# Performance work log

Hardware: AMD Instinct MI355X
Metric: run time of the kernel (lower is better)

## Reference

```python
import jax, jax.numpy as jnp
import numpy as np

B, S, D = 2, 2048, 1024
H, DK, DV = 16, 64, 64
DFF = 4096
EPS_RMS = 1e-6


def setup_inputs() -> dict:
    key = jax.random.key(0)
    ks = jax.random.split(key, 10)
    sc = 0.02
    return {
        "x": jax.random.normal(ks[0], (B, S, D), jnp.float32),
        "w_q": jax.random.normal(ks[1], (D, H * DK), jnp.float32) * sc,
        "w_k": jax.random.normal(ks[2], (D, H * DK), jnp.float32) * sc,
        "w_v": jax.random.normal(ks[3], (D, H * DV), jnp.float32) * sc,
        "w_o": jax.random.normal(ks[4], (H * DV, D), jnp.float32) * sc,
        "w_gate": jax.random.normal(ks[5], (D, DFF), jnp.float32) * sc,
        "w_up": jax.random.normal(ks[6], (D, DFF), jnp.float32) * sc,
        "w_down": jax.random.normal(ks[7], (DFF, D), jnp.float32) * sc,
        "g1": jnp.ones((D,), jnp.float32),
        "g2": jnp.ones((D,), jnp.float32),
    }


def _rmsnorm(x, g):
    var = jnp.mean(jnp.square(x), axis=-1, keepdims=True)
    return x * jax.lax.rsqrt(var + EPS_RMS) * g


def _stable_softmax(s):
    # Faithful to source: exp(x) / (sum exp(x) + 1e-9); fully-masked rows -> 0.
    e = jnp.exp(s)
    return e / (jnp.sum(e, axis=-1, keepdims=True) + 1e-9)


def reference(x, w_q, w_k, w_v, w_o, w_gate, w_up, w_down, g1, g2):
    b, s, d = x.shape
    h = _rmsnorm(x, g1)
    q = (h @ w_q).reshape(b, s, H, DK).transpose(0, 2, 1, 3)  # [B,H,S,DK]
    k = (h @ w_k).reshape(b, s, H, DK).transpose(0, 2, 1, 3)
    v = (h @ w_v).reshape(b, s, H, DV).transpose(0, 2, 1, 3)
    scores = jnp.einsum("bhqd,bhkd->bhqk", q, k) / jnp.sqrt(jnp.asarray(DK, x.dtype))
    # triu with diagonal=0: self and future positions are masked
    mask = jnp.triu(jnp.ones((s, s), bool))
    scores = jnp.where(mask, -jnp.inf, scores)
    attn = _stable_softmax(scores)  # [B,H,S,S]
    av = jnp.einsum("bhqk,bhkd->bhqd", attn, v)
    av = av.transpose(0, 2, 1, 3).reshape(b, s, H * DV)
    x = x + av @ w_o  # residual 1
    h2 = _rmsnorm(x, g2)
    hidden = jax.nn.silu(h2 @ w_gate) * (h2 @ w_up)
    return x + hidden @ w_down  # residual 2
```

## Files before the change

### kernel.cpp

```cpp
#include <hip/hip_runtime.h>
#include <cstdint>
#include <cstddef>

typedef unsigned short u16;
typedef unsigned char u8;
typedef unsigned int u32;
typedef __bf16 bf16x8 __attribute__((ext_vector_type(8)));
typedef float floatx4 __attribute__((ext_vector_type(4)));
typedef float floatx16 __attribute__((ext_vector_type(16)));
typedef int i32x8 __attribute__((ext_vector_type(8)));

#define B_ 2
#define S_ 2048
#define D_ 1024
#define H_ 16
#define DFF_ 4096
#define BS_ 4096

__device__ __forceinline__ u16 f2bf(float f) {
  u32 u = __builtin_bit_cast(u32, f);
  u += 0x7fffu + ((u >> 16) & 1u);
  return (u16)(u >> 16);
}
__device__ __forceinline__ float bf2f(u16 h) {
  u32 u = ((u32)h) << 16;
  return __builtin_bit_cast(float, u);
}

__device__ __forceinline__ u32 f2e4m3(float f) {
  u32 u = __builtin_bit_cast(u32, f);
  const u32 s = (u >> 24) & 0x80u;
  const u32 au = u & 0x7fffffffu;
  if (au < 0x3c800000u) return s;
  if (au > 0x43e00000u) return s | 0x7eu;
  const u32 lsb = (au >> 20) & 1u;
  const u32 r = au + 0x0007ffffu + lsb;
  const u32 e = (r >> 23) & 0xffu;
  const u32 m = (r >> 20) & 7u;
  return s | (((e - 120u) & 0xfu) << 3) | m;
}

__device__ __forceinline__ void gl_lds16(const void* g, void* l) {
  __builtin_amdgcn_global_load_lds(
      (const __attribute__((address_space(1))) void*)g,
      (__attribute__((address_space(3))) void*)l, 16, 0, 0);
}

__device__ __forceinline__ void xcd_swz(int GX, int GY, int& bx, int& by) {
  int flat = by * GX + bx;
  const int q = (GX * GY) >> 3;
  flat = (flat & 7) * q + (flat >> 3);
  bx = flat % GX;
  by = flat / GX;
}

__global__ void prep_weights(const float* __restrict__ wq, const float* __restrict__ wk,
                             const float* __restrict__ wv, const float* __restrict__ wo,
                             const float* __restrict__ wg, const float* __restrict__ wu,
                             const float* __restrict__ wd,
                             u16* __restrict__ wqkv_t, u16* __restrict__ wo_t,
                             u8* __restrict__ wguf8, u16* __restrict__ wdn_t) {
  __shared__ float tile[32][33];
  const int id = blockIdx.x;
  const float* src;
  u16* dst = nullptr;
  int R, C, bx, by, mode;
  if (id < 3072) {
    const int which = id >> 10, lo = id & 1023;
    src = which == 0 ? wq : (which == 1 ? wk : wv);
    dst = wqkv_t + which * 1024 * 1024;
    R = 1024; C = 1024; bx = lo & 31; by = lo >> 5; mode = 0;
  } else if (id < 4096) {
    const int lo = id - 3072;
    src = wo; dst = wo_t; R = 1024; C = 1024; bx = lo & 31; by = lo >> 5; mode = 0;
  } else if (id < 8192) {
    const int lo = id - 4096;
    src = wg; R = 1024; C = 4096; bx = lo & 127; by = lo >> 7; mode = 1;
  } else if (id < 12288) {
    const int lo = id - 8192;
    src = wu; R = 1024; C = 4096; bx = lo & 127; by = lo >> 7; mode = 2;
  } else {
    const int lo = id - 12288;
    src = wd; dst = wdn_t; R = 4096; C = 1024; bx = lo & 31; by = lo >> 5; mode = 0;
  }
  const int tx = threadIdx.x, ty = threadIdx.y;
  const int c0 = bx * 32, r0 = by * 32;
#pragma unroll
  for (int i = 0; i < 4; i++)
    tile[ty + i * 8][tx] = src[(size_t)(r0 + ty + i * 8) * C + c0 + tx];
  __syncthreads();
  const int sx = ty * 32 + tx;
  const int oci = sx >> 3, cg = (sx & 7) * 4;
  const int oc = c0 + oci;
  const float v0 = tile[cg][oci], v1 = tile[cg + 1][oci];
  const float v2 = tile[cg + 2][oci], v3 = tile[cg + 3][oci];
  if (mode == 0) {
    uint2 o;
    o.x = (u32)f2bf(v0) | ((u32)f2bf(v1) << 16);
    o.y = (u32)f2bf(v2) | ((u32)f2bf(v3) << 16);
    *(uint2*)(dst + (size_t)oc * R + r0 + cg) = o;
  } else {
    const int orow = (oc >> 5) * 64 + (oc & 31) + (mode == 2 ? 32 : 0);
    const u32 p = f2e4m3(v0 * 64.f) | (f2e4m3(v1 * 64.f) << 8) |
                  (f2e4m3(v2 * 64.f) << 16) | (f2e4m3(v3 * 64.f) << 24);
    *(u32*)(wguf8 + (size_t)orow * 1024 + r0 + cg) = p;
  }
}

template <int F8>
__global__ __launch_bounds__(256) void rmsnorm_kernel(const float* __restrict__ x,
                                                      const float* __restrict__ g,
                                                      void* __restrict__ out) {
  const int row = blockIdx.x, t = threadIdx.x;
  const float4 v = ((const float4*)(x + (size_t)row * 1024))[t];
  float ss = v.x * v.x + v.y * v.y + v.z * v.z + v.w * v.w;
#pragma unroll
  for (int off = 32; off > 0; off >>= 1) ss += __shfl_xor(ss, off);
  __shared__ float red[4];
  if ((t & 63) == 0) red[t >> 6] = ss;
  __syncthreads();
  ss = red[0] + red[1] + red[2] + red[3];
  const float inv = rsqrtf(ss * (1.0f / 1024.0f) + 1e-6f);
  const float4 gv = ((const float4*)g)[t];
  const float y0 = v.x * inv * gv.x, y1 = v.y * inv * gv.y;
  const float y2 = v.z * inv * gv.z, y3 = v.w * inv * gv.w;
  if (F8) {
    const u32 p = f2e4m3(y0) | (f2e4m3(y1) << 8) | (f2e4m3(y2) << 16) | (f2e4m3(y3) << 24);
    ((u32*)out)[(size_t)row * 256 + t] = p;
  } else {
    uint2 o;
    o.x = (u32)f2bf(y0) | ((u32)f2bf(y1) << 16);
    o.y = (u32)f2bf(y2) | ((u32)f2bf(y3) << 16);
    ((uint2*)out)[(size_t)row * 256 + t] = o;
  }
}

template <int BN>
__device__ __forceinline__ void bt_step(const u16* Asb, const u16* Bsb,
                                        floatx16 (&acc)[2][BN / 64],
                                        int wm, int wn, int c31, int khalf) {
  constexpr int NTI = BN / 64;
#pragma unroll
  for (int ks = 0; ks < 4; ks++) {
    bf16x8 af[2], bfr[NTI];
#pragma unroll
    for (int mi = 0; mi < 2; mi++) {
      const int row = wm * 64 + mi * 32 + c31;
      const int e = (ks * 2 + khalf) ^ (row & 7);
      af[mi] = *(const bf16x8*)(Asb + row * 64 + e * 8);
    }
#pragma unroll
    for (int ni = 0; ni < NTI; ni++) {
      const int row = wn * (BN / 2) + ni * 32 + c31;
      const int e = (ks * 2 + khalf) ^ (row & 7);
      bfr[ni] = *(const bf16x8*)(Bsb + row * 64 + e * 8);
    }
#pragma unroll
    for (int mi = 0; mi < 2; mi++)
#pragma unroll
      for (int ni = 0; ni < NTI; ni++)
        acc[mi][ni] = __builtin_amdgcn_mfma_f32_32x32x16_bf16(af[mi], bfr[ni],
                                                              acc[mi][ni], 0, 0, 0);
  }
}

template <int BN, int EPI, int PIPE>
__global__ __launch_bounds__(256) void gemm_bt(const u16* __restrict__ A,
                                               const u16* __restrict__ Bt,
                                               void* __restrict__ Cout,
                                               const float* __restrict__ res,
                                               u16* __restrict__ vTout,
                                               int M, int N, int K) {
  constexpr int NBUF = PIPE ? 2 : 1;
  __shared__ u16 As[NBUF][128 * 64];
  __shared__ u16 Bs[NBUF][BN * 64];
  constexpr int NTI = BN / 64;
  constexpr int NSEG = 16 + BN / 8;
  constexpr int SPW = NSEG / 4;
  const int t = threadIdx.x, w = t >> 6, l = t & 63;

  int bx = (int)blockIdx.x, by = (int)blockIdx.y;
  xcd_swz((int)gridDim.x, (int)gridDim.y, bx, by);
  const int m0 = by * 128, n0 = bx * BN;
  const int wm = w >> 1, wn = w & 1;
  const int c31 = l & 31, khalf = l >> 5;

  const u16* gsrc[SPW];
  u16* ld0[SPW];
  u16* ld1[SPW];
  {
    const int rl = l >> 3, ch = (l & 7) ^ rl;
#pragma unroll
    for (int i = 0; i < SPW; i++) {
      const int s = w * SPW + i;
      if (s < 16) {
        gsrc[i] = A + (size_t)(m0 + s * 8 + rl) * K + ch * 8;
        ld0[i] = As[0] + s * 512;
        ld1[i] = As[NBUF - 1] + s * 512;
      } else {
        gsrc[i] = Bt + (size_t)(n0 + (s - 16) * 8 + rl) * K + ch * 8;
        ld0[i] = Bs[0] + (s - 16) * 512;
        ld1[i] = Bs[NBUF - 1] + (s - 16) * 512;
      }
    }
  }

  floatx16 acc[2][NTI] = {};

  if constexpr (!PIPE) {
    for (int kk = 0; kk < K; kk += 64) {
      __syncthreads();
#pragma unroll
      for (int i = 0; i < SPW; i++) gl_lds16(gsrc[i], ld0[i]);
#pragma unroll
      for (int i = 0; i < SPW; i++) gsrc[i] += 64;
      __syncthreads();
      bt_step<BN>(As[0], Bs[0], acc, wm, wn, c31, khalf);
    }
  } else {
#pragma unroll
    for (int i = 0; i < SPW; i++) gl_lds16(gsrc[i], ld0[i]);
#pragma unroll
    for (int i = 0; i < SPW; i++) gsrc[i] += 64;
    asm volatile("s_waitcnt vmcnt(0)" ::: "memory");
    __builtin_amdgcn_s_barrier();
    for (int kk = 0; kk < K; kk += 128) {
#pragma unroll
      for (int i = 0; i < SPW; i++) gl_lds16(gsrc[i], ld1[i]);
#pragma unroll
      for (int i = 0; i < SPW; i++) gsrc[i] += 64;
      bt_step<BN>(As[0], Bs[0], acc, wm, wn, c31, khalf);
      asm volatile("s_waitcnt vmcnt(0)" ::: "memory");
      __builtin_amdgcn_s_barrier();
      if (kk + 128 < K) {
#pragma unroll
        for (int i = 0; i < SPW; i++) gl_lds16(gsrc[i], ld0[i]);
#pragma unroll
        for (int i = 0; i < SPW; i++) gsrc[i] += 64;
      }
      bt_step<BN>(As[NBUF - 1], Bs[NBUF - 1], acc, wm, wn, c31, khalf);
      asm volatile("s_waitcnt vmcnt(0)" ::: "memory");
      __builtin_amdgcn_s_barrier();
    }
  }

  if constexpr (EPI == 3) {
    if (n0 >= 2048) {
#pragma unroll
      for (int mi = 0; mi < 2; mi++)
#pragma unroll
        for (int ni = 0; ni < NTI; ni++) {
          const int col = n0 + wn * (BN / 2) + ni * 32 + c31 - 2048;
          const int hh = col >> 6, dv = col & 63;
          const int rbase = m0 + wm * 64 + mi * 32 + 4 * khalf;
          const int bb = rbase >> 11;
          u16* vp = vTout + (size_t)((bb * 16 + hh) * 64 + dv) * 2048 + (rbase & 2047);
#pragma unroll
          for (int rg = 0; rg < 4; rg++) {
            uint2 pk;
            pk.x = (u32)f2bf(acc[mi][ni][rg * 4 + 0]) |
                   ((u32)f2bf(acc[mi][ni][rg * 4 + 1]) << 16);
            pk.y = (u32)f2bf(acc[mi][ni][rg * 4 + 2]) |
                   ((u32)f2bf(acc[mi][ni][rg * 4 + 3]) << 16);
            *(uint2*)(vp + rg * 8) = pk;
          }
        }
      return;
    }
  }
#pragma unroll
  for (int mi = 0; mi < 2; mi++)
#pragma unroll
    for (int ni = 0; ni < NTI; ni++) {
      const int col = n0 + wn * (BN / 2) + ni * 32 + c31;
#pragma unroll
      for (int reg = 0; reg < 16; reg++) {
        const int row = m0 + wm * 64 + mi * 32 + (reg & 3) + 8 * (reg >> 2) + 4 * khalf;
        const size_t idx = (size_t)row * N + col;
        if (EPI == 1) ((float*)Cout)[idx] = acc[mi][ni][reg] + res[idx];
        else          ((u16*)Cout)[idx] = f2bf(acc[mi][ni][reg]);
      }
    }
}

__global__ __launch_bounds__(256) void gemm_f8(const u8* __restrict__ A,
                                               const u8* __restrict__ B,
                                               u16* __restrict__ hid,
                                               int M, int K) {
  __shared__ u8 As[128 * 64];
  __shared__ u8 Bs[128 * 64];
  const int t = threadIdx.x, w = t >> 6, l = t & 63;
  int bx = (int)blockIdx.x, by = (int)blockIdx.y;
  xcd_swz((int)gridDim.x, (int)gridDim.y, bx, by);
  const int m0 = by * 128, n0 = bx * 128;
  const int wm = w >> 1, wn = w & 1;
  const int c31 = l & 31, hf = l >> 5;

  const u8* gsrc[4];
  u8* ldst[4];
  {
    const int rl = l >> 2, ch = (l & 3) ^ ((l >> 3) & 3);
#pragma unroll
    for (int i = 0; i < 4; i++) {
      const int s = w * 4 + i;
      if (s < 8) {
        gsrc[i] = A + (size_t)(m0 + s * 16 + rl) * K + ch * 16;
        ldst[i] = As + s * 1024;
      } else {
        gsrc[i] = B + (size_t)(n0 + (s - 8) * 16 + rl) * K + ch * 16;
        ldst[i] = Bs + (s - 8) * 1024;
      }
    }
  }

  floatx16 acc[2][2] = {};

  for (int kk = 0; kk < K; kk += 64) {
    __syncthreads();
#pragma unroll
    for (int i = 0; i < 4; i++) gl_lds16(gsrc[i] + kk, ldst[i]);
    __syncthreads();

    i32x8 af[2], bf[2];
#pragma unroll
    for (int mi = 0; mi < 2; mi++) {
      const int r = wm * 64 + mi * 32 + c31;
      const int g = (r >> 1) & 3;
      const uint4 lo = *(const uint4*)(As + r * 64 + ((2 * hf) ^ g) * 16);
      const uint4 hi = *(const uint4*)(As + r * 64 + ((2 * hf + 1) ^ g) * 16);
      af[mi] = i32x8{(int)lo.x, (int)lo.y, (int)lo.z, (int)lo.w,
                     (int)hi.x, (int)hi.y, (int)hi.z, (int)hi.w};
    }
#pragma unroll
    for (int ni = 0; ni < 2; ni++) {
      const int r = wn * 64 + ni * 32 + c31;
      const int g = (r >> 1) & 3;
      const uint4 lo = *(const uint4*)(Bs + r * 64 + ((2 * hf) ^ g) * 16);
      const uint4 hi = *(const uint4*)(Bs + r * 64 + ((2 * hf + 1) ^ g) * 16);
      bf[ni] = i32x8{(int)lo.x, (int)lo.y, (int)lo.z, (int)lo.w,
                     (int)hi.x, (int)hi.y, (int)hi.z, (int)hi.w};
    }
#pragma unroll
    for (int mi = 0; mi < 2; mi++)
#pragma unroll
      for (int ni = 0; ni < 2; ni++)
        acc[mi][ni] = __builtin_amdgcn_mfma_scale_f32_32x32x64_f8f6f4(
            af[mi], bf[ni], acc[mi][ni], 0, 0,
            0, 0x7F7F7F7F,
            0, 0x79797979);
  }

#pragma unroll
  for (int mi = 0; mi < 2; mi++) {
    const int colo = (bx * 2 + wn) * 32 + c31;
#pragma unroll
    for (int reg = 0; reg < 16; reg++) {
      const int row = m0 + wm * 64 + mi * 32 + (reg & 3) + 8 * (reg >> 2) + 4 * hf;
      const float g = acc[mi][0][reg];
      const float u = acc[mi][1][reg];
      hid[(size_t)row * 4096 + colo] = f2bf(g / (1.f + __expf(-g)) * u);
    }
  }
}

__global__ __launch_bounds__(256) void attn_kernel(const u16* __restrict__ qkv,
                                                   const u16* __restrict__ vT,
                                                   u16* __restrict__ av) {
  __shared__ u16 SM[2 * 8192];
  __shared__ u16 Ps[4 * 2048];
  const int t = threadIdx.x, w = t >> 6, l = t & 63;
  const int lrow = l & 15, lk = l >> 4;
  const int bh = blockIdx.x;
  const int b = bh >> 4, h = bh & 15;
  const int qt = 15 - (int)blockIdx.y;
  const int qbase = qt * 128 + w * 32;
  const int ktmax = 2 * qt + 1;
  u16* Pw = Ps + w * 2048;

  bf16x8 aq[2][2];
#pragma unroll
  for (int sub = 0; sub < 2; sub++)
#pragma unroll
    for (int half = 0; half < 2; half++)
      aq[sub][half] = *(const bf16x8*)(qkv + (size_t)(b * S_ + qbase + sub * 16 + lrow) * 3072 +
                                       h * 64 + half * 32 + lk * 8);

  const u16* gcur[4];
  int gstep[4], loff[4];
#pragma unroll
  for (int i = 0; i < 4; i++) {
    const int c = w + 4 * i;
    const int half = (c >> 2) & 1, grp = c & 3;
    if (c < 8) {
      gcur[i] = qkv + (size_t)(b * S_ + grp * 16 + (l >> 2)) * 3072 + D_ + h * 64 +
                half * 32 + (l & 3) * 8;
      gstep[i] = 64 * 3072;
      loff[i] = half * 2048 + grp * 512;
    } else {
      gcur[i] = vT + (size_t)(bh * 64 + grp * 16 + (l >> 2)) * S_ + half * 32 + (l & 3) * 8;
      gstep[i] = 64;
      loff[i] = 4096 + half * 2048 + grp * 512;
    }
  }

  floatx4 oacc[2][4] = {};
  float den[2] = {0.f, 0.f};

  int cur = 0;
#pragma unroll
  for (int i = 0; i < 4; i++) { gl_lds16(gcur[i], SM + loff[i]); gcur[i] += gstep[i]; }

  for (int kt = 0; kt <= ktmax; kt++) {
    __syncthreads();
    if (kt < ktmax) {
#pragma unroll
      for (int i = 0; i < 4; i++) {
        gl_lds16(gcur[i], SM + (cur ^ 1) * 8192 + loff[i]);
        gcur[i] += gstep[i];
      }
    }
    const u16* Kbuf = SM + cur * 8192;
    const u16* Vbuf = Kbuf + 4096;

    bf16x8 bk[4][2];
#pragma unroll
    for (int ct = 0; ct < 4; ct++)
#pragma unroll
      for (int half = 0; half < 2; half++)
        bk[ct][half] = *(const bf16x8*)(Kbuf + half * 2048 + (ct * 16 + lrow) * 32 + lk * 8);

    floatx4 sf[2][4] = {};
#pragma unroll
    for (int sub = 0; sub < 2; sub++)
#pragma unroll
      for (int ct = 0; ct < 4; ct++) {
        sf[sub][ct] = __builtin_amdgcn_mfma_f32_16x16x32_bf16(bk[ct][0], aq[sub][0],
                                                              sf[sub][ct], 0, 0, 0);
        sf[sub][ct] = __builtin_amdgcn_mfma_f32_16x16x32_bf16(bk[ct][1], aq[sub][1],
                                                              sf[sub][ct], 0, 0, 0);
      }

#pragma unroll
    for (int sub = 0; sub < 2; sub++) {
      const int qp = qbase + sub * 16 + lrow;
      const int prow = sub * 16 + lrow;
#pragma unroll
      for (int ct = 0; ct < 4; ct++) {
        const int kb = kt * 64 + ct * 16 + lk * 4;
        float p0 = (kb + 0 < qp) ? __expf(sf[sub][ct][0] * 0.125f) : 0.f;
        float p1 = (kb + 1 < qp) ? __expf(sf[sub][ct][1] * 0.125f) : 0.f;
        float p2 = (kb + 2 < qp) ? __expf(sf[sub][ct][2] * 0.125f) : 0.f;
        float p3 = (kb + 3 < qp) ? __expf(sf[sub][ct][3] * 0.125f) : 0.f;
        den[sub] += (p0 + p1) + (p2 + p3);
        uint2 pk;
        pk.x = (u32)f2bf(p0) | ((u32)f2bf(p1) << 16);
        pk.y = (u32)f2bf(p2) | ((u32)f2bf(p3) << 16);
        *(uint2*)(Pw + prow * 64 + (((2 * ct + (lk >> 1)) ^ (lrow & 7)) << 3) +
                  (lk & 1) * 4) = pk;
      }
    }

    bf16x8 ap[2][2], bv[4][2];
#pragma unroll
    for (int sub = 0; sub < 2; sub++)
#pragma unroll
      for (int kh = 0; kh < 2; kh++) {
        const int prow = sub * 16 + lrow;
        ap[sub][kh] = *(const bf16x8*)(Pw + prow * 64 + (((kh * 4 + lk) ^ (prow & 7)) << 3));
      }
#pragma unroll
    for (int ni = 0; ni < 4; ni++)
#pragma unroll
      for (int kh = 0; kh < 2; kh++)
        bv[ni][kh] = *(const bf16x8*)(Vbuf + kh * 2048 + (ni * 16 + lrow) * 32 + lk * 8);
#pragma unroll
    for (int sub = 0; sub < 2; sub++)
#pragma unroll
      for (int ni = 0; ni < 4; ni++) {
        oacc[sub][ni] = __builtin_amdgcn_mfma_f32_16x16x32_bf16(ap[sub][0], bv[ni][0],
                                                                oacc[sub][ni], 0, 0, 0);
        oacc[sub][ni] = __builtin_amdgcn_mfma_f32_16x16x32_bf16(ap[sub][1], bv[ni][1],
                                                                oacc[sub][ni], 0, 0, 0);
      }
    cur ^= 1;
  }

#pragma unroll
  for (int sub = 0; sub < 2; sub++) {
    den[sub] += __shfl_xor(den[sub], 16);
    den[sub] += __shfl_xor(den[sub], 32);
  }
  float dq[2][4];
#pragma unroll
  for (int sub = 0; sub < 2; sub++)
#pragma unroll
    for (int r = 0; r < 4; r++)
      dq[sub][r] = __shfl(den[sub], lk * 4 + r);

#pragma unroll
  for (int sub = 0; sub < 2; sub++)
#pragma unroll
    for (int ni = 0; ni < 4; ni++)
#pragma unroll
      for (int r = 0; r < 4; r++) {
        const int row = qbase + sub * 16 + lk * 4 + r;
        const int col = h * 64 + ni * 16 + lrow;
        av[(size_t)(b * S_ + row) * 1024 + col] = f2bf(oacc[sub][ni][r] / (dq[sub][r] + 1e-9f));
      }
}

#define OFF_WQKV 0u
#define OFF_WO   6291456u
#define OFF_WGU8 8388608u
#define OFF_WDN  16777216u
#define OFF_H1   25165824u
#define OFF_QKV  33554432u
#define OFF_VT   58720256u
#define OFF_AV   67108864u
#define OFF_X1   75497472u
#define OFF_H2F8 92274688u
#define OFF_HID  96468992u

extern "C" void kernel_launch(void* const* d_in, const int* in_sizes, int n_in,
                              void* d_out, int out_size, void* d_ws, size_t ws_size,
                              hipStream_t stream) {
  const float* x      = (const float*)d_in[0];
  const float* w_q    = (const float*)d_in[1];
  const float* w_k    = (const float*)d_in[2];
  const float* w_v    = (const float*)d_in[3];
  const float* w_o    = (const float*)d_in[4];
  const float* w_gate = (const float*)d_in[5];
  const float* w_up   = (const float*)d_in[6];
  const float* w_down = (const float*)d_in[7];
  const float* g1     = (const float*)d_in[8];
  const float* g2     = (const float*)d_in[9];

  char* ws = (char*)d_ws;
  u16* wqkv_t = (u16*)(ws + OFF_WQKV);
  u16* wo_t   = (u16*)(ws + OFF_WO);
  u8*  wguf8  = (u8*)(ws + OFF_WGU8);
  u16* wdn_t  = (u16*)(ws + OFF_WDN);
  u16* h1     = (u16*)(ws + OFF_H1);
  u16* qkv    = (u16*)(ws + OFF_QKV);
  u16* vT     = (u16*)(ws + OFF_VT);
  u16* av     = (u16*)(ws + OFF_AV);
  float* x1   = (float*)(ws + OFF_X1);
  u8*  h2f8   = (u8*)(ws + OFF_H2F8);
  u16* hid    = (u16*)(ws + OFF_HID);
  float* out  = (float*)d_out;

  prep_weights<<<16384, dim3(32, 8), 0, stream>>>(w_q, w_k, w_v, w_o, w_gate, w_up, w_down,
                                                  wqkv_t, wo_t, wguf8, wdn_t);

  rmsnorm_kernel<0><<<BS_, 256, 0, stream>>>(x, g1, h1);
  gemm_bt<128, 3, 0><<<dim3(3072 / 128, BS_ / 128), 256, 0, stream>>>(
      h1, wqkv_t, qkv, nullptr, vT, BS_, 3072, 1024);
  attn_kernel<<<dim3(32, 16), 256, 0, stream>>>(qkv, vT, av);
  gemm_bt<64, 1, 1><<<dim3(1024 / 64, BS_ / 128), 256, 0, stream>>>(
      av, wo_t, x1, x, nullptr, BS_, 1024, 1024);
  rmsnorm_kernel<1><<<BS_, 256, 0, stream>>>(x1, g2, h2f8);
  gemm_f8<<<dim3(4096 / 64, BS_ / 128), 256, 0, stream>>>(h2f8, wguf8, hid, BS_, 1024);
  gemm_bt<64, 1, 1><<<dim3(1024 / 64, BS_ / 128), 256, 0, stream>>>(
      hid, wdn_t, out, x1, nullptr, BS_, 1024, 4096);
}
```

Before: 342.2 us.

## Double-buffer FP8 GEMM, skip masked attention tiles, use exp2 and packed bf16

The FP8 gate/up GEMM now uses two LDS buffers, so the global-to-LDS load of the next K slice overlaps the MFMA work on the current one, with explicit waitcnt and barriers. In the attention kernel, each wave skips key tiles that lie entirely in its masked region. The mask comparison runs only on diagonal tiles, exp is replaced by a raw v_exp_f32 with the log2(e) factor folded into the scale, and the bf16 packing uses v_cvt_pk_bf16_f32; s_setprio is raised around the MFMA blocks. The QKV GEMM launch switches to a narrower 64-column tile and a different template mode, which changes occupancy and the wave count. The extra LDS for double buffering may reduce occupancy, and the QKV template change could alter the epilogue path.

```diff
diff --git a/kernel.cpp b/kernel.cpp
--- a/kernel.cpp
+++ b/kernel.cpp
@@ -25,6 +25,18 @@
 __device__ __forceinline__ float bf2f(u16 h) {
   u32 u = ((u32)h) << 16;
   return __builtin_bit_cast(float, u);
+}
+
+__device__ __forceinline__ u32 cvtpk_bf16(float lo, float hi) {
+  u32 r;
+  asm("v_cvt_pk_bf16_f32 %0, %1, %2" : "=v"(r) : "v"(lo), "v"(hi));
+  return r;
+}
+
+__device__ __forceinline__ float fexp2(float x) {
+  float r;
+  asm("v_exp_f32 %0, %1" : "=v"(r) : "v"(x));
+  return r;
 }
 
 __device__ __forceinline__ u32 f2e4m3(float f) {
@@ -283,12 +295,44 @@
     }
 }
 
+__device__ __forceinline__ void f8_step(const u8* Asb, const u8* Bsb,
+                                        floatx16 (&acc)[2][2],
+                                        int wm, int wn, int c31, int hf) {
+  i32x8 af[2], bf[2];
+#pragma unroll
+  for (int mi = 0; mi < 2; mi++) {
+    const int r = wm * 64 + mi * 32 + c31;
+    const int g = (r >> 1) & 3;
+    const uint4 lo = *(const uint4*)(Asb + r * 64 + ((2 * hf) ^ g) * 16);
+    const uint4 hi = *(const uint4*)(Asb + r * 64 + ((2 * hf + 1) ^ g) * 16);
+    af[mi] = i32x8{(int)lo.x, (int)lo.y, (int)lo.z, (int)lo.w,
+                   (int)hi.x, (int)hi.y, (int)hi.z, (int)hi.w};
+  }
+#pragma unroll
+  for (int ni = 0; ni < 2; ni++) {
+    const int r = wn * 64 + ni * 32 + c31;
+    const int g = (r >> 1) & 3;
+    const uint4 lo = *(const uint4*)(Bsb + r * 64 + ((2 * hf) ^ g) * 16);
+    const uint4 hi = *(const uint4*)(Bsb + r * 64 + ((2 * hf + 1) ^ g) * 16);
+    bf[ni] = i32x8{(int)lo.x, (int)lo.y, (int)lo.z, (int)lo.w,
+                   (int)hi.x, (int)hi.y, (int)hi.z, (int)hi.w};
+  }
+#pragma unroll
+  for (int mi = 0; mi < 2; mi++)
+#pragma unroll
+    for (int ni = 0; ni < 2; ni++)
+      acc[mi][ni] = __builtin_amdgcn_mfma_scale_f32_32x32x64_f8f6f4(
+          af[mi], bf[ni], acc[mi][ni], 0, 0,
+          0, 0x7F7F7F7F,
+          0, 0x79797979);
+}
+
 __global__ __launch_bounds__(256) void gemm_f8(const u8* __restrict__ A,
                                                const u8* __restrict__ B,
                                                u16* __restrict__ hid,
                                                int M, int K) {
-  __shared__ u8 As[128 * 64];
-  __shared__ u8 Bs[128 * 64];
+  __shared__ u8 As[2][128 * 64];
+  __shared__ u8 Bs[2][128 * 64];
   const int t = threadIdx.x, w = t >> 6, l = t & 63;
   int bx = (int)blockIdx.x, by = (int)blockIdx.y;
   xcd_swz((int)gridDim.x, (int)gridDim.y, bx, by);
@@ -297,7 +341,8 @@
   const int c31 = l & 31, hf = l >> 5;
 
   const u8* gsrc[4];
-  u8* ldst[4];
+  u8* ld0[4];
+  u8* ld1[4];
   {
     const int rl = l >> 2, ch = (l & 3) ^ ((l >> 3) & 3);
 #pragma unroll
@@ -305,49 +350,35 @@
       const int s = w * 4 + i;
       if (s < 8) {
         gsrc[i] = A + (size_t)(m0 + s * 16 + rl) * K + ch * 16;
-        ldst[i] = As + s * 1024;
+        ld0[i] = As[0] + s * 1024;
+        ld1[i] = As[1] + s * 1024;
       } else {
         gsrc[i] = B + (size_t)(n0 + (s - 8) * 16 + rl) * K + ch * 16;
-        ldst[i] = Bs + (s - 8) * 1024;
+        ld0[i] = Bs[0] + (s - 8) * 1024;
+        ld1[i] = Bs[1] + (s - 8) * 1024;
       }
     }
   }
 
   floatx16 acc[2][2] = {};
 
-  for (int kk = 0; kk < K; kk += 64) {
-    __syncthreads();
-#pragma unroll
-    for (int i = 0; i < 4; i++) gl_lds16(gsrc[i] + kk, ldst[i]);
-    __syncthreads();
-
-    i32x8 af[2], bf[2];
-#pragma unroll
-    for (int mi = 0; mi < 2; mi++) {
-      const int r = wm * 64 + mi * 32 + c31;
-      const int g = (r >> 1) & 3;
-      const uint4 lo = *(const uint4*)(As + r * 64 + ((2 * hf) ^ g) * 16);
-      const uint4 hi = *(const uint4*)(As + r * 64 + ((2 * hf + 1) ^ g) * 16);
-      af[mi] = i32x8{(int)lo.x, (int)lo.y, (int)lo.z, (int)lo.w,
-                     (int)hi.x, (int)hi.y, (int)hi.z, (int)hi.w};
-    }
-#pragma unroll
-    for (int ni = 0; ni < 2; ni++) {
-      const int r = wn * 64 + ni * 32 + c31;
-      const int g = (r >> 1) & 3;
-      const uint4 lo = *(const uint4*)(Bs + r * 64 + ((2 * hf) ^ g) * 16);
-      const uint4 hi = *(const uint4*)(Bs + r * 64 + ((2 * hf + 1) ^ g) * 16);
-      bf[ni] = i32x8{(int)lo.x, (int)lo.y, (int)lo.z, (int)lo.w,
-                     (int)hi.x, (int)hi.y, (int)hi.z, (int)hi.w};
-    }
-#pragma unroll
-    for (int mi = 0; mi < 2; mi++)
-#pragma unroll
-      for (int ni = 0; ni < 2; ni++)
-        acc[mi][ni] = __builtin_amdgcn_mfma_scale_f32_32x32x64_f8f6f4(
-            af[mi], bf[ni], acc[mi][ni], 0, 0,
-            0, 0x7F7F7F7F,
-            0, 0x79797979);
+#pragma unroll
+  for (int i = 0; i < 4; i++) gl_lds16(gsrc[i], ld0[i]);
+  asm volatile("s_waitcnt vmcnt(0)" ::: "memory");
+  __builtin_amdgcn_s_barrier();
+  for (int kk = 0; kk < K; kk += 128) {
+#pragma unroll
+    for (int i = 0; i < 4; i++) gl_lds16(gsrc[i] + kk + 64, ld1[i]);
+    f8_step(As[0], Bs[0], acc, wm, wn, c31, hf);
+    asm volatile("s_waitcnt vmcnt(0)" ::: "memory");
+    __builtin_amdgcn_s_barrier();
+    if (kk + 128 < K) {
+#pragma unroll
+      for (int i = 0; i < 4; i++) gl_lds16(gsrc[i] + kk + 128, ld0[i]);
+    }
+    f8_step(As[1], Bs[1], acc, wm, wn, c31, hf);
+    asm volatile("s_waitcnt vmcnt(0)" ::: "memory");
+    __builtin_amdgcn_s_barrier();
   }
 
 #pragma unroll
@@ -376,6 +407,7 @@
   const int qbase = qt * 128 + w * 32;
   const int ktmax = 2 * qt + 1;
   u16* Pw = Ps + w * 2048;
+  const float SC = 0.125f * 1.44269504088896f;
 
   bf16x8 aq[2][2];
 #pragma unroll
@@ -422,66 +454,95 @@
     const u16* Kbuf = SM + cur * 8192;
     const u16* Vbuf = Kbuf + 4096;
 
-    bf16x8 bk[4][2];
-#pragma unroll
-    for (int ct = 0; ct < 4; ct++)
-#pragma unroll
-      for (int half = 0; half < 2; half++)
-        bk[ct][half] = *(const bf16x8*)(Kbuf + half * 2048 + (ct * 16 + lrow) * 32 + lk * 8);
-
-    floatx4 sf[2][4] = {};
-#pragma unroll
-    for (int sub = 0; sub < 2; sub++)
-#pragma unroll
-      for (int ct = 0; ct < 4; ct++) {
-        sf[sub][ct] = __builtin_amdgcn_mfma_f32_16x16x32_bf16(bk[ct][0], aq[sub][0],
-                                                              sf[sub][ct], 0, 0, 0);
-        sf[sub][ct] = __builtin_amdgcn_mfma_f32_16x16x32_bf16(bk[ct][1], aq[sub][1],
-                                                              sf[sub][ct], 0, 0, 0);
+    const bool active = (kt * 64 < qbase + 31);
+    if (active) {
+      const bool need_mask = (kt * 64 + 64 > qbase);
+
+      bf16x8 bk[4][2];
+#pragma unroll
+      for (int ct = 0; ct < 4; ct++)
+#pragma unroll
+        for (int half = 0; half < 2; half++)
+          bk[ct][half] = *(const bf16x8*)(Kbuf + half * 2048 + (ct * 16 + lrow) * 32 + lk * 8);
+
+      floatx4 sf[2][4] = {};
+      __builtin_amdgcn_s_setprio(1);
+#pragma unroll
+      for (int sub = 0; sub < 2; sub++)
+#pragma unroll
+        for (int ct = 0; ct < 4; ct++) {
+          sf[sub][ct] = __builtin_amdgcn_mfma_f32_16x16x32_bf16(bk[ct][0], aq[sub][0],
+                                                                sf[sub][ct], 0, 0, 0);
+          sf[sub][ct] = __builtin_amdgcn_mfma_f32_16x16x32_bf16(bk[ct][1], aq[sub][1],
+                                                                sf[sub][ct], 0, 0, 0);
+        }
+      __builtin_amdgcn_s_setprio(0);
+
+      if (!need_mask) {
+#pragma unroll
+        for (int sub = 0; sub < 2; sub++) {
+          const int prow = sub * 16 + lrow;
+#pragma unroll
+          for (int ct = 0; ct < 4; ct++) {
+            const float p0 = fexp2(sf[sub][ct][0] * SC);
+            const float p1 = fexp2(sf[sub][ct][1] * SC);
+            const float p2 = fexp2(sf[sub][ct][2] * SC);
+            const float p3 = fexp2(sf[sub][ct][3] * SC);
+            den[sub] += (p0 + p1) + (p2 + p3);
+            uint2 pk;
+            pk.x = cvtpk_bf16(p0, p1);
+            pk.y = cvtpk_bf16(p2, p3);
+            *(uint2*)(Pw + prow * 64 + (((2 * ct + (lk >> 1)) ^ (lrow & 7)) << 3) +
+                      (lk & 1) * 4) = pk;
+          }
+        }
+      } else {
+#pragma unroll
+        for (int sub = 0; sub < 2; sub++) {
+          const int qp = qbase + sub * 16 + lrow;
+          const int prow = sub * 16 + lrow;
+#pragma unroll
+          for (int ct = 0; ct < 4; ct++) {
+            const int kb = kt * 64 + ct * 16 + lk * 4;
+            const float p0 = (kb + 0 < qp) ? fexp2(sf[sub][ct][0] * SC) : 0.f;
+            const float p1 = (kb + 1 < qp) ? fexp2(sf[sub][ct][1] * SC) : 0.f;
+            const float p2 = (kb + 2 < qp) ? fexp2(sf[sub][ct][2] * SC) : 0.f;
+            const float p3 = (kb + 3 < qp) ? fexp2(sf[sub][ct][3] * SC) : 0.f;
+            den[sub] += (p0 + p1) + (p2 + p3);
+            uint2 pk;
+            pk.x = cvtpk_bf16(p0, p1);
+            pk.y = cvtpk_bf16(p2, p3);
+            *(uint2*)(Pw + prow * 64 + (((2 * ct + (lk >> 1)) ^ (lrow & 7)) << 3) +
+                      (lk & 1) * 4) = pk;
+          }
+        }
       }
 
-#pragma unroll
-    for (int sub = 0; sub < 2; sub++) {
-      const int qp = qbase + sub * 16 + lrow;
-      const int prow = sub * 16 + lrow;
-#pragma unroll
-      for (int ct = 0; ct < 4; ct++) {
-        const int kb = kt * 64 + ct * 16 + lk * 4;
-        float p0 = (kb + 0 < qp) ? __expf(sf[sub][ct][0] * 0.125f) : 0.f;
-        float p1 = (kb + 1 < qp) ? __expf(sf[sub][ct][1] * 0.125f) : 0.f;
-        float p2 = (kb + 2 < qp) ? __expf(sf[sub][ct][2] * 0.125f) : 0.f;
-        float p3 = (kb + 3 < qp) ? __expf(sf[sub][ct][3] * 0.125f) : 0.f;
-        den[sub] += (p0 + p1) + (p2 + p3);
-        uint2 pk;
-        pk.x = (u32)f2bf(p0) | ((u32)f2bf(p1) << 16);
-        pk.y = (u32)f2bf(p2) | ((u32)f2bf(p3) << 16);
-        *(uint2*)(Pw + prow * 64 + (((2 * ct + (lk >> 1)) ^ (lrow & 7)) << 3) +
-                  (lk & 1) * 4) = pk;
-      }
-    }
-
-    bf16x8 ap[2][2], bv[4][2];
-#pragma unroll
-    for (int sub = 0; sub < 2; sub++)
-#pragma unroll
-      for (int kh = 0; kh < 2; kh++) {
-        const int prow = sub * 16 + lrow;
-        ap[sub][kh] = *(const bf16x8*)(Pw + prow * 64 + (((kh * 4 + lk) ^ (prow & 7)) << 3));
-      }
-#pragma unroll
-    for (int ni = 0; ni < 4; ni++)
-#pragma unroll
-      for (int kh = 0; kh < 2; kh++)
-        bv[ni][kh] = *(const bf16x8*)(Vbuf + kh * 2048 + (ni * 16 + lrow) * 32 + lk * 8);
-#pragma unroll
-    for (int sub = 0; sub < 2; sub++)
-#pragma unroll
-      for (int ni = 0; ni < 4; ni++) {
-        oacc[sub][ni] = __builtin_amdgcn_mfma_f32_16x16x32_bf16(ap[sub][0], bv[ni][0],
-                                                                oacc[sub][ni], 0, 0, 0);
-        oacc[sub][ni] = __builtin_amdgcn_mfma_f32_16x16x32_bf16(ap[sub][1], bv[ni][1],
-                                                                oacc[sub][ni], 0, 0, 0);
-      }
+      bf16x8 ap[2][2], bv[4][2];
+#pragma unroll
+      for (int sub = 0; sub < 2; sub++)
+#pragma unroll
+        for (int kh = 0; kh < 2; kh++) {
+          const int prow = sub * 16 + lrow;
+          ap[sub][kh] = *(const bf16x8*)(Pw + prow * 64 + (((kh * 4 + lk) ^ (prow & 7)) << 3));
+        }
+#pragma unroll
+      for (int ni = 0; ni < 4; ni++)
+#pragma unroll
+        for (int kh = 0; kh < 2; kh++)
+          bv[ni][kh] = *(const bf16x8*)(Vbuf + kh * 2048 + (ni * 16 + lrow) * 32 + lk * 8);
+      __builtin_amdgcn_s_setprio(1);
+#pragma unroll
+      for (int sub = 0; sub < 2; sub++)
+#pragma unroll
+        for (int ni = 0; ni < 4; ni++) {
+          oacc[sub][ni] = __builtin_amdgcn_mfma_f32_16x16x32_bf16(ap[sub][0], bv[ni][0],
+                                                                  oacc[sub][ni], 0, 0, 0);
+          oacc[sub][ni] = __builtin_amdgcn_mfma_f32_16x16x32_bf16(ap[sub][1], bv[ni][1],
+                                                                  oacc[sub][ni], 0, 0, 0);
+        }
+      __builtin_amdgcn_s_setprio(0);
+    }
     cur ^= 1;
   }
 
@@ -553,7 +614,7 @@
                                                   wqkv_t, wo_t, wguf8, wdn_t);
 
   rmsnorm_kernel<0><<<BS_, 256, 0, stream>>>(x, g1, h1);
-  gemm_bt<128, 3, 0><<<dim3(3072 / 128, BS_ / 128), 256, 0, stream>>>(
+  gemm_bt<64, 3, 1><<<dim3(3072 / 64, BS_ / 128), 256, 0, stream>>>(
       h1, wqkv_t, qkv, nullptr, vT, BS_, 3072, 1024);
   attn_kernel<<<dim3(32, 16), 256, 0, stream>>>(qkv, vT, av);
   gemm_bt<64, 1, 1><<<dim3(1024 / 64, BS_ / 128), 256, 0, stream>>>(
```

Result: no change. 344.5 us (+0.7%).
